# Kernel tuning notes

Measured on AMD Instinct MI355X. Metric: run time of the kernel, lower is better.

The kernel has to match this reference:

```python
import jax, jax.numpy as jnp
import numpy as np

N_U, N_I, N_B, D, L = 100000, 50000, 10, 64, 2
N_EDGES, BATCH = 1000000, 2048
DROPOUT, TEMP = 0.25, 0.2
LAMBDA_1, LAMBDA_2, LAMBDA_3 = 0.2, 0.2, 1e-7
IS_NORM = True


def setup_inputs() -> dict:
    key = jax.random.key(0)
    ks = jax.random.split(key, 10)
    E_u_0 = jax.random.normal(ks[0], (N_U, D), jnp.float32) * 0.01
    E_v_0 = jax.random.normal(ks[1], (N_I, D), jnp.float32) * 0.01
    E_b = jax.random.normal(ks[2], (N_B, D), jnp.float32) * 0.01
    adj_vals = jax.random.uniform(ks[3], (N_EDGES,), jnp.float32) * 0.05
    adj_rows = jax.random.randint(ks[4], (N_EDGES,), 0, N_U, jnp.int32)
    adj_cols = jax.random.randint(ks[5], (N_EDGES,), 0, N_I, jnp.int32)
    uids = jax.random.randint(ks[6], (BATCH,), 0, N_U, jnp.int32)
    iids = jax.random.randint(ks[7], (BATCH,), 0, N_I, jnp.int32)
    pos = jax.random.randint(ks[8], (BATCH,), 0, N_I, jnp.int32)
    neg = jax.random.randint(ks[9], (BATCH,), 0, N_I, jnp.int32)
    return {"E_u_0": E_u_0, "E_v_0": E_v_0, "E_b": E_b, "adj_vals": adj_vals,
            "adj_rows": adj_rows, "adj_cols": adj_cols,
            "uids": uids, "iids": iids, "pos": pos, "neg": neg}


def _sparse_dropout(key, vals):
    # fresh Bernoulli mask + inverted-dropout rescale on the sparse values
    keep = jax.random.bernoulli(key, 1.0 - DROPOUT, vals.shape)
    return jnp.where(keep, vals / (1.0 - DROPOUT), jnp.zeros_like(vals))


def _propagate(Eu0, Ev0, vals, rows, cols, base_key):
    # L layers of bipartite spmm: Eu <- A @ Ev ; Ev <- A.T @ Eu (fresh dropout each spmm)
    Eu, Ev = Eu0, Ev0
    Eu_sum, Ev_sum = Eu0, Ev0
    for layer in range(L):
        v1 = _sparse_dropout(jax.random.fold_in(base_key, 2 * layer), vals)
        v2 = _sparse_dropout(jax.random.fold_in(base_key, 2 * layer + 1), vals)
        Eu_new = jax.ops.segment_sum(v1[:, None] * Ev[cols], rows, num_segments=Eu0.shape[0])
        Ev_new = jax.ops.segment_sum(v2[:, None] * Eu[rows], cols, num_segments=Ev0.shape[0])
        Eu, Ev = Eu_new, Ev_new
        Eu_sum = Eu_sum + Eu
        Ev_sum = Ev_sum + Ev
    return Eu_sum, Ev_sum


def reference(E_u_0, E_v_0, E_b, adj_vals, adj_rows, adj_cols, uids, iids, pos, neg):
    drop_key = jax.random.key(42)
    # base graph propagation
    E_u, E_v = _propagate(E_u_0, E_v_0, adj_vals, adj_rows, adj_cols,
                          jax.random.fold_in(drop_key, 0))
    # learned edge weights -> augmented graph (detached, elementwise * adj_norm)
    edge_logits = jnp.sum(E_u[adj_rows] * E_v[adj_cols], axis=1)  # [E]
    Ag = jax.nn.sigmoid(edge_logits)
    aug_vals = jax.lax.stop_gradient(Ag) * adj_vals
    Z_u, Z_i = _propagate(E_u_0, E_v_0, aug_vals, adj_rows, adj_cols,
                          jax.random.fold_in(drop_key, 1))
    # BPR loss
    u_emb, pos_emb, neg_emb = E_u[uids], E_v[pos], E_v[neg]
    pos_scores = jnp.sum(u_emb * pos_emb, axis=-1)
    neg_scores = jnp.sum(u_emb * neg_emb, axis=-1)
    loss_bpr = -jnp.mean(jnp.log(jax.nn.sigmoid(pos_scores - neg_scores)))
    # PCL (InfoNCE between augmented and base views)
    neg_s = jnp.mean(jnp.log(jnp.sum(jnp.exp(Z_u[uids] @ E_u.T / TEMP), axis=1) + 1e-8))
    neg_s = neg_s + jnp.mean(jnp.log(jnp.sum(jnp.exp(Z_i[iids] @ E_v.T / TEMP), axis=1) + 1e-8))
    pos_s = jnp.mean(jnp.clip(jnp.sum(Z_u[uids] * E_u[uids], axis=1) / TEMP, -5.0, 5.0))
    pos_s = pos_s + jnp.mean(jnp.clip(jnp.sum(Z_i[iids] * E_v[iids], axis=1) / TEMP, -5.0, 5.0))
    loss_pcl = neg_s - pos_s
    # BCL (bucketed contrastive loss; is_norm=True, is_mean=False)
    if IS_NORM:
        weight_b = (pos_scores - pos_scores.min()) / (pos_scores.max() - pos_scores.min() + 1e-9)
    else:
        weight_b = jax.nn.sigmoid(pos_scores)
    relations = jnp.clip((weight_b * N_B).astype(jnp.int32), 0, N_B - 1)  # [B]
    el = jax.nn.sigmoid(E_u[uids] * E_v[pos])                              # [B, D]
    xb = E_b[relations]                                                    # [B, D]
    mask = 1.0 - jax.nn.one_hot(relations, N_B, dtype=el.dtype)            # [B, N_B]
    neg_bcl = jnp.mean(jnp.mean((el @ E_b.T) * mask, axis=-1))
    pos_bcl = jnp.mean(jnp.sum(el * xb, axis=-1))
    loss_bcl = neg_bcl - pos_bcl
    # L2 reg over parameters
    loss_reg = LAMBDA_3 * (jnp.sum(E_u_0 ** 2) + jnp.sum(E_v_0 ** 2) + jnp.sum(E_b ** 2))
    loss = loss_bpr + LAMBDA_1 * loss_pcl + LAMBDA_2 * loss_bcl + loss_reg
    return jnp.stack([loss, loss_bpr, LAMBDA_1 * loss_pcl, LAMBDA_2 * loss_bcl])
```

## Files before the change

### kernel.cpp

```cpp
#include <hip/hip_runtime.h>
#include <stdint.h>

#define NU 100000
#define NI 50000
#define NBK 10
#define DD 64
#define NE 1000000
#define BATCH 2048
#define NSLICE 8
#define USLICE ((NU + NSLICE - 1) / NSLICE)
#define ISLICE ((NI + NSLICE - 1) / NSLICE)
#define NCHUNK 512
#define EPC ((NE + NCHUNK - 1) / NCHUNK)
#define CAP_U 32
#define CAP_I 64
#define FP8_SCALE 128.0f
#define SPMM_DESCALE (1.0f / 96.0f)
#define EL_DESCALE (1.0f / 16384.0f)
#define LOG2E5 7.2134752f
#define AV_ENC 40960.0f
#define AV_DEC (0.05f / 2048.0f)
#define AUG_ENC (65535.0f / 0.05f)
#define AUG_DEC (0.05f / 65535.0f)

typedef __bf16 bf16x8 __attribute__((ext_vector_type(8)));
typedef float f32x4 __attribute__((ext_vector_type(4)));
typedef float f32x2 __attribute__((ext_vector_type(2)));
typedef unsigned long long u64x2 __attribute__((ext_vector_type(2)));

struct Keys8 { uint32_t k[8][2]; };

__host__ __device__ inline void tf2x32(uint32_t k0, uint32_t k1, uint32_t x0, uint32_t x1,
                                       uint32_t& o0, uint32_t& o1) {
  uint32_t ks0 = k0, ks1 = k1, ks2 = k0 ^ k1 ^ 0x1BD11BDAu;
  x0 += ks0; x1 += ks1;
#define TFR(r) { x0 += x1; x1 = (x1 << (r)) | (x1 >> (32 - (r))); x1 ^= x0; }
  TFR(13) TFR(15) TFR(26) TFR(6)   x0 += ks1; x1 += ks2 + 1u;
  TFR(17) TFR(29) TFR(16) TFR(24)  x0 += ks2; x1 += ks0 + 2u;
  TFR(13) TFR(15) TFR(26) TFR(6)   x0 += ks0; x1 += ks1 + 3u;
  TFR(17) TFR(29) TFR(16) TFR(24)  x0 += ks1; x1 += ks2 + 4u;
  TFR(13) TFR(15) TFR(26) TFR(6)   x0 += ks2; x1 += ks0 + 5u;
#undef TFR
  o0 = x0; o1 = x1;
}

__device__ inline uint16_t f2bf(float f) {
  uint32_t u = __float_as_uint(f);
  return (uint16_t)((u + 0x7fffu + ((u >> 16) & 1u)) >> 16);
}
__device__ inline float bf2f(uint16_t u) {
  return __uint_as_float(((uint32_t)u) << 16);
}

__device__ inline uint32_t mm_enc(float f) {
  uint32_t s = __float_as_uint(f);
  return (s & 0x80000000u) ? ~s : (s | 0x80000000u);
}
__device__ inline float mm_dec(uint32_t u) {
  uint32_t s = (u & 0x80000000u) ? (u ^ 0x80000000u) : ~u;
  return __uint_as_float(s);
}

template <int SEL>
__device__ inline float fp8_sel(uint32_t w) {
#if __has_builtin(__builtin_amdgcn_cvt_f32_fp8)
  return __builtin_amdgcn_cvt_f32_fp8((int)w, SEL);
#else
  uint32_t b = (w >> (8 * SEL)) & 0xFFu;
  uint32_t s = b >> 7, e = (b >> 3) & 0xF, m = b & 7;
  float v = (e == 0) ? (float)m * (1.0f / 512.0f)
                     : __uint_as_float(((e + 120) << 23) | (m << 20));
  return s ? -v : v;
#endif
}
__device__ inline f32x4 fp8_to4(uint32_t w) {
#if __has_builtin(__builtin_amdgcn_cvt_pk_f32_fp8)
  f32x2 lo = __builtin_amdgcn_cvt_pk_f32_fp8((int)w, false);
  f32x2 hi = __builtin_amdgcn_cvt_pk_f32_fp8((int)w, true);
  f32x4 r; r[0] = lo[0]; r[1] = lo[1]; r[2] = hi[0]; r[3] = hi[1];
  return r;
#else
  f32x4 r; r[0] = fp8_sel<0>(w); r[1] = fp8_sel<1>(w);
  r[2] = fp8_sel<2>(w); r[3] = fp8_sel<3>(w);
  return r;
#endif
}
__device__ inline uint32_t f32_to_fp8(float f) {
#if __has_builtin(__builtin_amdgcn_cvt_pk_fp8_f32)
  return (uint32_t)__builtin_amdgcn_cvt_pk_fp8_f32(f, f, 0, false) & 0xFFu;
#else
  uint32_t s = (__float_as_uint(f) >> 31) << 7;
  float a = fabsf(f);
  a = fminf(a, 448.0f);
  if (a < 0.015625f) {
    uint32_t m = (uint32_t)(a * 512.0f + 0.5f);
    return s | m;
  }
  int ex; float fr = frexpf(a, &ex);
  uint32_t q = (uint32_t)(fr * 16.0f + 0.5f);
  int E = ex + 6;
  if (q == 16) { q = 8; E += 1; }
  if (E > 15) { E = 15; q = 14; }
  if (E == 15 && q == 15) q = 14;
  return s | ((uint32_t)E << 3) | (q - 8);
#endif
}
__device__ inline uint32_t pack4_fp8(float a, float b, float c, float d) {
  return f32_to_fp8(a) | (f32_to_fp8(b) << 8) | (f32_to_fp8(c) << 16) | (f32_to_fp8(d) << 24);
}

__device__ inline uint64_t pack_edge(int r, int c, uint32_t m, float a) {
  uint32_t q = (uint32_t)(a * AV_ENC + 0.5f);
  if (q > 2047u) q = 2047u;
  return (uint64_t)(uint32_t)r | ((uint64_t)(uint32_t)c << 17) |
         ((uint64_t)m << 33) | ((uint64_t)q << 41);
}

#define CVTB 2048
#define MASKB ((NE / 2 + 255) / 256)
#define ZEROB ((NU + NI + 255) / 256)

__global__ void prep_kernel(const float4* __restrict__ a, int na4,
                            uint32_t* __restrict__ oca, uint32_t* __restrict__ oia,
                            const float4* __restrict__ b, int nb4,
                            uint32_t* __restrict__ ocb, uint32_t* __restrict__ oib,
                            const float4* __restrict__ c, int nc4,
                            float* __restrict__ acc,
                            const int* __restrict__ rows, const int* __restrict__ cols,
                            const float* __restrict__ av,
                            uint64_t* __restrict__ pk, Keys8 K,
                            int* __restrict__ cnt, uint32_t* __restrict__ mmi) {
  int bid = blockIdx.x, tid = threadIdx.x;
  if (bid < CVTB) {
    __shared__ float red[256];
    int total = na4 + nb4 + nc4;
    float s = 0.f;
    for (int i = bid * 256 + tid; i < total; i += CVTB * 256) {
      float4 v = (i < na4) ? a[i] : (i < na4 + nb4) ? b[i - na4] : c[i - na4 - nb4];
      s += v.x * v.x + v.y * v.y + v.z * v.z + v.w * v.w;
      if (i < na4 + nb4) {
        uint32_t w = pack4_fp8(v.x * FP8_SCALE, v.y * FP8_SCALE, v.z * FP8_SCALE, v.w * FP8_SCALE);
        if (i < na4) {
          oca[i] = w;
          oia[((i >> 4) << 5) + ((i & 15) << 1)] = w;
        } else {
          int j = i - na4;
          ocb[j] = w;
          oib[((j >> 4) << 5) + ((j & 15) << 1)] = w;
        }
      }
    }
    red[tid] = s;
    __syncthreads();
    for (int st = 128; st > 0; st >>= 1) {
      if (tid < st) red[tid] += red[tid + st];
      __syncthreads();
    }
    if (tid == 0) atomicAdd(&acc[7], red[0]);
  } else if (bid < CVTB + MASKB) {
    const int half = NE / 2;
    int e = (bid - CVTB) * 256 + tid;
    if (e >= half) return;
    uint32_t mlo = 0, mhi = 0;
#pragma unroll
    for (int j = 0; j < 8; ++j) {
      uint32_t o0, o1;
      tf2x32(K.k[j][0], K.k[j][1], (uint32_t)e, (uint32_t)(e + half), o0, o1);
      float u0 = __uint_as_float((o0 >> 9) | 0x3f800000u) - 1.0f;
      float u1 = __uint_as_float((o1 >> 9) | 0x3f800000u) - 1.0f;
      mlo |= (u0 < 0.75f ? 1u : 0u) << j;
      mhi |= (u1 < 0.75f ? 1u : 0u) << j;
    }
    pk[e] = pack_edge(rows[e], cols[e], mlo, av[e]);
    pk[e + half] = pack_edge(rows[e + half], cols[e + half], mhi, av[e + half]);
  } else {
    int i = (bid - CVTB - MASKB) * 256 + tid;
    if (i < NU + NI) cnt[i] = 0;
    if (i == 0) { mmi[0] = 0xFFFFFFFFu; mmi[1] = 0u; }
  }
}

__global__ __launch_bounds__(256)
void scatter_kernel(const uint64_t* __restrict__ pk,
                    int* __restrict__ cntU, int* __restrict__ cntI,
                    int* __restrict__ cpU, int* __restrict__ cpI) {
  int slice = blockIdx.x & 7;
  int chunk = blockIdx.x >> 3;
  int base = chunk * EPC;
  int end = base + EPC; if (end > NE) end = NE;
  for (int e = base + 2 * (int)threadIdx.x; e < end; e += 512) {
    u64x2 pp = __builtin_nontemporal_load((const u64x2*)(pk + e));
    uint64_t p0 = pp[0], p1 = pp[1];
    int r0 = (int)(p0 & 0x1FFFFu), r1 = (int)(p1 & 0x1FFFFu);
    int c0 = (int)((p0 >> 17) & 0xFFFFu), c1 = (int)((p1 >> 17) & 0xFFFFu);
    uint32_t m0 = (uint32_t)(p0 >> 33) & 0xFFu, m1 = (uint32_t)(p1 >> 33) & 0xFFu;
    uint32_t q0 = ((uint32_t)(p0 >> 41) & 0x7FFu) << 21;
    uint32_t q1 = ((uint32_t)(p1 >> 41) & 0x7FFu) << 21;
    if (r0 / USLICE == slice) {
      int old = atomicAdd(&cntU[r0], 1);
      cpU[(r0 << 5) + old] = (int)((uint32_t)c0 | ((m0 & 0xFu) << 17) | q0);
    }
    if (r1 / USLICE == slice) {
      int old = atomicAdd(&cntU[r1], 1);
      cpU[(r1 << 5) + old] = (int)((uint32_t)c1 | ((m1 & 0xFu) << 17) | q1);
    }
    if (c0 / ISLICE == slice) {
      int old = atomicAdd(&cntI[c0], 1);
      cpI[(c0 << 6) + old] = (int)((uint32_t)r0 | (((m0 >> 4) & 0xFu) << 17) | q0);
    }
    if (c1 / ISLICE == slice) {
      int old = atomicAdd(&cntI[c1], 1);
      cpI[(c1 << 6) + old] = (int)((uint32_t)r1 | (((m1 >> 4) & 0xFu) << 17) | q1);
    }
  }
}

__device__ inline float cp_weight(int cc, const uint16_t* __restrict__ rdw, int p, int shift) {
  float mb = (float)((cc >> shift) & 1);
  if (rdw) return (float)rdw[p] * AUG_DEC * mb;
  return (float)(((uint32_t)cc) >> 21) * AV_DEC * mb;
}

__global__ __launch_bounds__(256)
void spmm_layer_kernel(const int* __restrict__ cntU, const int* __restrict__ cpU,
                       const int* __restrict__ cntI, const int* __restrict__ cpI,
                       const uint16_t* __restrict__ rdU, const uint16_t* __restrict__ rdI,
                       int shift,
                       const uint8_t* __restrict__ SU, const uint8_t* __restrict__ SI,
                       uint8_t* __restrict__ dU, uint8_t* __restrict__ dI,
                       uint16_t* __restrict__ sumU, uint16_t* __restrict__ sumI,
                       const float* __restrict__ baseU, const float* __restrict__ baseI,
                       uint8_t* __restrict__ s8U, uint8_t* __restrict__ s8I) {
  int lane = threadIdx.x & 63;
  int g = lane >> 4, l15 = lane & 15;
  int w = (blockIdx.x * blockDim.x + threadIdx.x) >> 6;
  int r = w * 4 + g;
  const int* cnt; const int* cp; const uint8_t* S; const uint16_t* rdw;
  uint8_t* D; uint16_t* Sum; const float* base; uint8_t* S8; int row, cap;
  if (r < NU) {
    row = r; cnt = cntU; cp = cpU; S = SU; rdw = rdU; cap = CAP_U;
    D = dU; Sum = sumU; base = baseU; S8 = s8U;
  } else {
    row = r - NU; cnt = cntI; cp = cpI; S = SI; rdw = rdI; cap = CAP_I;
    D = dI; Sum = sumI; base = baseI; S8 = s8I;
  }
  int p0 = row * cap, p1 = p0 + cnt[row];
  f32x4 acc = {0.f, 0.f, 0.f, 0.f};
  int p = p0;
  for (; p + 4 <= p1; p += 4) {
    int c0 = cp[p], c1 = cp[p + 1], c2 = cp[p + 2], c3 = cp[p + 3];
    float v0 = cp_weight(c0, rdw, p, shift);
    float v1 = cp_weight(c1, rdw, p + 1, shift);
    float v2 = cp_weight(c2, rdw, p + 2, shift);
    float v3 = cp_weight(c3, rdw, p + 3, shift);
    uint32_t a0 = (v0 != 0.f) ? (uint32_t)(c0 & 0x1FFFF) : 0u;
    uint32_t a1 = (v1 != 0.f) ? (uint32_t)(c1 & 0x1FFFF) : 0u;
    uint32_t a2 = (v2 != 0.f) ? (uint32_t)(c2 & 0x1FFFF) : 0u;
    uint32_t a3 = (v3 != 0.f) ? (uint32_t)(c3 & 0x1FFFF) : 0u;
    uint32_t w0 = *(const uint32_t*)(S + ((size_t)a0 << 6) + l15 * 4);
    uint32_t w1 = *(const uint32_t*)(S + ((size_t)a1 << 6) + l15 * 4);
    uint32_t w2 = *(const uint32_t*)(S + ((size_t)a2 << 6) + l15 * 4);
    uint32_t w3 = *(const uint32_t*)(S + ((size_t)a3 << 6) + l15 * 4);
    f32x4 f0 = fp8_to4(w0), f1 = fp8_to4(w1), f2 = fp8_to4(w2), f3 = fp8_to4(w3);
#pragma unroll
    for (int k = 0; k < 4; ++k)
      acc[k] += (v0 * f0[k] + v1 * f1[k]) + (v2 * f2[k] + v3 * f3[k]);
  }
  for (; p < p1; ++p) {
    int c0 = cp[p];
    float v0 = cp_weight(c0, rdw, p, shift);
    if (v0 != 0.f) {
      uint32_t w0 = *(const uint32_t*)(S + ((size_t)(uint32_t)(c0 & 0x1FFFF) << 6) + l15 * 4);
      f32x4 f0 = fp8_to4(w0);
#pragma unroll
      for (int k = 0; k < 4; ++k) acc[k] += v0 * f0[k];
    }
  }
  size_t idx = (size_t)row * DD + l15 * 4;
  if (D) {
    *(uint32_t*)(D + idx) = pack4_fp8(acc[0] * (4.0f / 3.0f), acc[1] * (4.0f / 3.0f),
                                      acc[2] * (4.0f / 3.0f), acc[3] * (4.0f / 3.0f));
    float4 b4 = *(const float4*)(base + idx);
    ushort4 s;
    s.x = f2bf(b4.x + acc[0] * SPMM_DESCALE);
    s.y = f2bf(b4.y + acc[1] * SPMM_DESCALE);
    s.z = f2bf(b4.z + acc[2] * SPMM_DESCALE);
    s.w = f2bf(b4.w + acc[3] * SPMM_DESCALE);
    *(ushort4*)(Sum + idx) = s;
  } else {
    ushort4 s = *(const ushort4*)(Sum + idx);
    float s0 = bf2f(s.x) + acc[0] * SPMM_DESCALE;
    float s1 = bf2f(s.y) + acc[1] * SPMM_DESCALE;
    float s2 = bf2f(s.z) + acc[2] * SPMM_DESCALE;
    float s3 = bf2f(s.w) + acc[3] * SPMM_DESCALE;
    s.x = f2bf(s0); s.y = f2bf(s1); s.z = f2bf(s2); s.w = f2bf(s3);
    *(ushort4*)(Sum + idx) = s;
    if (S8)
      *(uint32_t*)(S8 + ((size_t)row << 7) + l15 * 8 + 4) =
          pack4_fp8(s0 * FP8_SCALE, s1 * FP8_SCALE, s2 * FP8_SCALE, s3 * FP8_SCALE);
  }
}

__global__ __launch_bounds__(256)
void spmm_aug_kernel(const int* __restrict__ cntU, const int* __restrict__ cpU,
                     const int* __restrict__ cntI, const int* __restrict__ cpI,
                     const uint8_t* __restrict__ TU, const uint8_t* __restrict__ TI,
                     uint8_t* __restrict__ dU, uint8_t* __restrict__ dI,
                     uint16_t* __restrict__ sumU, uint16_t* __restrict__ sumI,
                     const float* __restrict__ baseU, const float* __restrict__ baseI,
                     uint16_t* __restrict__ wrU, uint16_t* __restrict__ wrI) {
  int lane = threadIdx.x & 63;
  int g = lane >> 4, l15 = lane & 15;
  int w = (blockIdx.x * blockDim.x + threadIdx.x) >> 6;
  int r = w * 4 + g;
  const int* cnt; const int* cp; const uint8_t *T, *Rt;
  uint8_t* D; uint16_t* Sum; const float* base; uint16_t* wr; int row, cap;
  if (r < NU) {
    row = r; cnt = cntU; cp = cpU; T = TI; Rt = TU; cap = CAP_U;
    D = dU; Sum = sumU; base = baseU; wr = wrU;
  } else {
    row = r - NU; cnt = cntI; cp = cpI; T = TU; Rt = TI; cap = CAP_I;
    D = dI; Sum = sumI; base = baseI; wr = wrI;
  }
  uint32_t rv = *(const uint32_t*)(Rt + ((size_t)row << 7) + l15 * 8 + 4);
  f32x4 rr = fp8_to4(rv);
  int p0 = row * cap, p1 = p0 + cnt[row];
  f32x4 acc = {0.f, 0.f, 0.f, 0.f};
  int p = p0;
  for (; p + 4 <= p1; p += 4) {
    int c0 = cp[p], c1 = cp[p + 1], c2 = cp[p + 2], c3 = cp[p + 3];
    uint2 sg0 = *(const uint2*)(T + ((size_t)(uint32_t)(c0 & 0x1FFFF) << 7) + l15 * 8);
    uint2 sg1 = *(const uint2*)(T + ((size_t)(uint32_t)(c1 & 0x1FFFF) << 7) + l15 * 8);
    uint2 sg2 = *(const uint2*)(T + ((size_t)(uint32_t)(c2 & 0x1FFFF) << 7) + l15 * 8);
    uint2 sg3 = *(const uint2*)(T + ((size_t)(uint32_t)(c3 & 0x1FFFF) << 7) + l15 * 8);
    f32x4 g0 = fp8_to4(sg0.y), g1 = fp8_to4(sg1.y);
    f32x4 g2 = fp8_to4(sg2.y), g3 = fp8_to4(sg3.y);
    float d0 = rr[0] * g0[0] + rr[1] * g0[1] + rr[2] * g0[2] + rr[3] * g0[3];
    float d1 = rr[0] * g1[0] + rr[1] * g1[1] + rr[2] * g1[2] + rr[3] * g1[3];
    float d2 = rr[0] * g2[0] + rr[1] * g2[1] + rr[2] * g2[2] + rr[3] * g2[3];
    float d3 = rr[0] * g3[0] + rr[1] * g3[1] + rr[2] * g3[2] + rr[3] * g3[3];
#pragma unroll
    for (int o = 1; o < 16; o <<= 1) {
      d0 += __shfl_xor(d0, o, 16);
      d1 += __shfl_xor(d1, o, 16);
      d2 += __shfl_xor(d2, o, 16);
      d3 += __shfl_xor(d3, o, 16);
    }
    float a0 = (float)(((uint32_t)c0) >> 21) * AV_DEC / (1.0f + __expf(-d0 * EL_DESCALE));
    float a1 = (float)(((uint32_t)c1) >> 21) * AV_DEC / (1.0f + __expf(-d1 * EL_DESCALE));
    float a2 = (float)(((uint32_t)c2) >> 21) * AV_DEC / (1.0f + __expf(-d2 * EL_DESCALE));
    float a3 = (float)(((uint32_t)c3) >> 21) * AV_DEC / (1.0f + __expf(-d3 * EL_DESCALE));
    if (l15 == 0) {
      wr[p] = (uint16_t)(a0 * AUG_ENC + 0.5f);
      wr[p + 1] = (uint16_t)(a1 * AUG_ENC + 0.5f);
      wr[p + 2] = (uint16_t)(a2 * AUG_ENC + 0.5f);
      wr[p + 3] = (uint16_t)(a3 * AUG_ENC + 0.5f);
    }
    float v0 = a0 * (float)((c0 >> 19) & 1);
    float v1 = a1 * (float)((c1 >> 19) & 1);
    float v2 = a2 * (float)((c2 >> 19) & 1);
    float v3 = a3 * (float)((c3 >> 19) & 1);
    f32x4 f0 = fp8_to4(sg0.x), f1 = fp8_to4(sg1.x);
    f32x4 f2 = fp8_to4(sg2.x), f3 = fp8_to4(sg3.x);
#pragma unroll
    for (int k = 0; k < 4; ++k)
      acc[k] += (v0 * f0[k] + v1 * f1[k]) + (v2 * f2[k] + v3 * f3[k]);
  }
  for (; p < p1; ++p) {
    int c0 = cp[p];
    uint2 sg0 = *(const uint2*)(T + ((size_t)(uint32_t)(c0 & 0x1FFFF) << 7) + l15 * 8);
    f32x4 g0 = fp8_to4(sg0.y);
    float d0 = rr[0] * g0[0] + rr[1] * g0[1] + rr[2] * g0[2] + rr[3] * g0[3];
#pragma unroll
    for (int o = 1; o < 16; o <<= 1) d0 += __shfl_xor(d0, o, 16);
    float a0 = (float)(((uint32_t)c0) >> 21) * AV_DEC / (1.0f + __expf(-d0 * EL_DESCALE));
    if (l15 == 0) wr[p] = (uint16_t)(a0 * AUG_ENC + 0.5f);
    float v0 = a0 * (float)((c0 >> 19) & 1);
    f32x4 f0 = fp8_to4(sg0.x);
#pragma unroll
    for (int k = 0; k < 4; ++k) acc[k] += v0 * f0[k];
  }
  size_t idx = (size_t)row * DD + l15 * 4;
  *(uint32_t*)(D + idx) = pack4_fp8(acc[0] * (4.0f / 3.0f), acc[1] * (4.0f / 3.0f),
                                    acc[2] * (4.0f / 3.0f), acc[3] * (4.0f / 3.0f));
  float4 b4 = *(const float4*)(base + idx);
  ushort4 s;
  s.x = f2bf(b4.x + acc[0] * SPMM_DESCALE);
  s.y = f2bf(b4.y + acc[1] * SPMM_DESCALE);
  s.z = f2bf(b4.z + acc[2] * SPMM_DESCALE);
  s.w = f2bf(b4.w + acc[3] * SPMM_DESCALE);
  *(ushort4*)(Sum + idx) = s;
}

__global__ __launch_bounds__(256)
void pcl_mfma9_kernel(const uint16_t* __restrict__ Zgu, const uint16_t* __restrict__ E16u,
                      int NTu, float* __restrict__ Su,
                      const uint16_t* __restrict__ Zgi, const uint16_t* __restrict__ E16i,
                      int NTi, float* __restrict__ Si) {
  __shared__ uint8_t ldsb[2][2048];
  int lane = threadIdx.x & 63;
  int wave = threadIdx.x >> 6;
  int quad = lane >> 4, l15 = lane & 15;
  bool isU = blockIdx.y < 8;
  const uint16_t* Zg = isU ? Zgu : Zgi;
  const uint16_t* E16 = isU ? E16u : E16i;
  int NT = isU ? NTu : NTi;
  float* S = isU ? Su : Si;
  const int SPL = 128;
  int mt0 = (((int)blockIdx.y & 7) * 4 + wave) * 4;
  bf16x8 a0[4], a1[4];
#pragma unroll
  for (int i = 0; i < 4; ++i) {
    const uint16_t* ar = Zg + (size_t)((mt0 + i) * 16 + l15) * 64 + quad * 8;
    a0[i] = *(const bf16x8*)ar;
    a1[i] = *(const bf16x8*)(ar + 32);
  }
  int t = threadIdx.x;
  int wof = (t * 8) ^ (((t >> 4) & 7) << 4);
  int rof0 = (l15 * 128 + quad * 16) ^ ((l15 & 7) << 4);
  int rof1 = (l15 * 128 + quad * 16 + 64) ^ ((l15 & 7) << 4);
  f32x4 rs[4] = {};
  int nt = blockIdx.x;
  {
    uint2 g0 = make_uint2(0u, 0u);
    if (nt < NT)
      g0 = *(const uint2*)((const uint8_t*)E16 + (size_t)nt * 2048 + t * 8);
    *(uint2*)(&ldsb[0][wof]) = g0;
  }
  __syncthreads();
  int cur = 0;
  while (nt < NT) {
    int nn = nt + SPL;
    uint2 gn = make_uint2(0u, 0u);
    if (nn < NT)
      gn = *(const uint2*)((const uint8_t*)E16 + (size_t)nn * 2048 + t * 8);
    bf16x8 b0 = *(const bf16x8*)(&ldsb[cur][rof0]);
    bf16x8 b1 = *(const bf16x8*)(&ldsb[cur][rof1]);
#pragma unroll
    for (int i = 0; i < 4; ++i) {
      f32x4 c = {0.f, 0.f, 0.f, 0.f};
      c = __builtin_amdgcn_mfma_f32_16x16x32_bf16(a0[i], b0, c, 0, 0, 0);
      c = __builtin_amdgcn_mfma_f32_16x16x32_bf16(a1[i], b1, c, 0, 0, 0);
#pragma unroll
      for (int r = 0; r < 4; ++r) rs[i][r] += __builtin_amdgcn_exp2f(c[r]);
    }
    *(uint2*)(&ldsb[cur ^ 1][wof]) = gn;
    __syncthreads();
    cur ^= 1; nt = nn;
  }
#pragma unroll
  for (int off = 8; off > 0; off >>= 1) {
#pragma unroll
    for (int i = 0; i < 4; ++i)
#pragma unroll
      for (int r = 0; r < 4; ++r) rs[i][r] += __shfl_down(rs[i][r], off, 16);
  }
  if (l15 == 0) {
#pragma unroll
    for (int i = 0; i < 4; ++i)
#pragma unroll
      for (int r = 0; r < 4; ++r)
        atomicAdd(&S[(mt0 + i) * 16 + quad * 4 + r], rs[i][r]);
  }
}

__global__ __launch_bounds__(256)
void post_kernel(const uint16_t* __restrict__ Z16u, const uint16_t* __restrict__ Z16i,
                 const uint16_t* __restrict__ E16u, const uint16_t* __restrict__ E16i,
                 const int* __restrict__ uids, const int* __restrict__ iids,
                 const int* __restrict__ pos, const int* __restrict__ neg,
                 uint16_t* __restrict__ Zgu, uint16_t* __restrict__ Zgi,
                 float* __restrict__ ps, float* __restrict__ acc,
                 uint32_t* __restrict__ mmi) {
  int bid = blockIdx.x, tid = threadIdx.x;
  int lane = tid & 63;
  if (bid < 1024) {
    int row = bid * 4 + (tid >> 6);
    if (row < BATCH)
      Zgu[(size_t)row * 64 + lane] = f2bf(bf2f(Z16u[(size_t)uids[row] * 64 + lane]) * LOG2E5);
    else {
      int bb = row - BATCH;
      Zgi[(size_t)bb * 64 + lane] = f2bf(bf2f(Z16i[(size_t)iids[bb] * 64 + lane]) * LOG2E5);
    }
  } else if (bid < 1536) {
    int b = ((bid - 1024) * 256 + tid) >> 6;
    if (b >= BATCH) return;
    float u = bf2f(E16u[(size_t)uids[b] * DD + lane]);
    float p = u * bf2f(E16i[(size_t)pos[b] * DD + lane]);
    float n = u * bf2f(E16i[(size_t)neg[b] * DD + lane]);
#pragma unroll
    for (int off = 32; off > 0; off >>= 1) { p += __shfl_down(p, off); n += __shfl_down(n, off); }
    if (lane == 0) {
      ps[b] = p;
      uint32_t eu = mm_enc(p);
      atomicMin(&mmi[0], eu);
      atomicMax(&mmi[1], eu);
      float x = p - n;
      atomicAdd(&acc[0], logf(1.0f / (1.0f + __expf(-x))));
    }
  } else {
    int b = ((bid - 1536) * 256 + tid) >> 6;
    if (b >= 2 * BATCH) return;
    const uint16_t *Z, *E; const int* ids; int idx, bb;
    if (b < BATCH) { Z = Z16u; E = E16u; ids = uids; idx = 3; bb = b; }
    else { Z = Z16i; E = E16i; ids = iids; idx = 4; bb = b - BATCH; }
    size_t r = (size_t)ids[bb] * DD + lane;
    float p = bf2f(Z[r]) * bf2f(E[r]);
#pragma unroll
    for (int off = 32; off > 0; off >>= 1) p += __shfl_down(p, off);
    if (lane == 0) {
      float x = p * 5.0f;
      x = fminf(5.0f, fmaxf(-5.0f, x));
      atomicAdd(&acc[idx], x);
    }
  }
}

__global__ void bcl_kernel(const uint16_t* __restrict__ E16u, const uint16_t* __restrict__ E16i,
                           const float* __restrict__ Eb, const int* __restrict__ uids,
                           const int* __restrict__ pos, const float* __restrict__ ps,
                           const uint32_t* __restrict__ mmi, float* __restrict__ acc) {
  int lane = threadIdx.x & 63;
  int b = (blockIdx.x * blockDim.x + threadIdx.x) >> 6;
  if (b >= BATCH) return;
  float mn = mm_dec(mmi[0]);
  float mx = mm_dec(mmi[1]);
  float wgt = (ps[b] - mn) / (mx - mn + 1e-9f);
  int rel = (int)(wgt * 10.0f);
  rel = rel < 0 ? 0 : (rel > 9 ? 9 : rel);
  float x = bf2f(E16u[(size_t)uids[b] * DD + lane]) * bf2f(E16i[(size_t)pos[b] * DD + lane]);
  float el = 1.0f / (1.0f + __expf(-x));
  float sneg = 0.f, spos = 0.f;
  for (int k = 0; k < NBK; ++k) {
    float d = el * Eb[k * DD + lane];
#pragma unroll
    for (int off = 32; off > 0; off >>= 1) d += __shfl_down(d, off);
    if (lane == 0) { if (k == rel) spos = d; else sneg += d; }
  }
  if (lane == 0) {
    atomicAdd(&acc[5], sneg * 0.1f);
    atomicAdd(&acc[6], spos);
  }
}

__global__ void finalize_kernel(const float* __restrict__ Su, const float* __restrict__ Si,
                                const float* __restrict__ acc, float* __restrict__ out) {
  __shared__ float r1[256], r2[256];
  int tid = threadIdx.x;
  float su = 0.f, si = 0.f;
  for (int b = tid; b < BATCH; b += 256) {
    su += logf(Su[b] + 1e-8f);
    si += logf(Si[b] + 1e-8f);
  }
  r1[tid] = su; r2[tid] = si;
  __syncthreads();
  for (int s = 128; s > 0; s >>= 1) {
    if (tid < s) { r1[tid] += r1[tid + s]; r2[tid] += r2[tid + s]; }
    __syncthreads();
  }
  if (tid == 0) {
    const float inv = 1.0f / (float)BATCH;
    float neg_s = (r1[0] + r2[0]) * inv;
    float pos_s = (acc[3] + acc[4]) * inv;
    float pcl = neg_s - pos_s;
    float bpr = -acc[0] * inv;
    float bcl = (acc[5] - acc[6]) * inv;
    float reg = 1e-7f * acc[7];
    float loss = bpr + 0.2f * pcl + 0.2f * bcl + reg;
    out[0] = loss; out[1] = bpr; out[2] = 0.2f * pcl; out[3] = 0.2f * bcl;
  }
}

extern "C" void kernel_launch(void* const* d_in, const int* in_sizes, int n_in,
                              void* d_out, int out_size, void* d_ws, size_t ws_size,
                              hipStream_t stream) {
  (void)in_sizes; (void)n_in; (void)out_size; (void)ws_size;
  const float* Eu0 = (const float*)d_in[0];
  const float* Ev0 = (const float*)d_in[1];
  const float* Eb  = (const float*)d_in[2];
  const float* av  = (const float*)d_in[3];
  const int* rows  = (const int*)d_in[4];
  const int* cols  = (const int*)d_in[5];
  const int* uids  = (const int*)d_in[6];
  const int* iids  = (const int*)d_in[7];
  const int* pos   = (const int*)d_in[8];
  const int* neg   = (const int*)d_in[9];
  float* out = (float*)d_out;

  float* w = (float*)d_ws;
  size_t o = 0;
  float* ps  = w + o; o += BATCH;
  float* Su  = w + o; o += BATCH;
  float* Si  = w + o; o += BATCH;
  float* acc = w + o; o += 16;
  uint32_t* mmi = (uint32_t*)(w + o); o += 2;
  uint16_t* hp = (uint16_t*)(w + o);
  uint16_t* E16u = hp; hp += (size_t)NU * DD;
  uint16_t* E16i = hp; hp += (size_t)NI * DD;
  uint16_t* Z16u = hp; hp += (size_t)NU * DD;
  uint16_t* Z16i = hp; hp += (size_t)NI * DD;
  uint16_t* Zgu  = hp; hp += (size_t)BATCH * DD;
  uint16_t* Zgi  = hp; hp += (size_t)BATCH * DD;
  uint16_t* augU = hp; hp += (size_t)NU * CAP_U + 64;
  uint16_t* augI = hp; hp += (size_t)NI * CAP_I + 64;
  uint8_t* bp = (uint8_t*)hp;
  uint8_t* TU  = bp; bp += (size_t)NU * 128;
  uint8_t* TI  = bp; bp += (size_t)NI * 128;
  uint8_t* E0u8 = bp; bp += (size_t)NU * DD;
  uint8_t* E0v8 = bp; bp += (size_t)NI * DD;
  uint8_t* d8U = bp; bp += (size_t)NU * DD;
  uint8_t* d8I = bp; bp += (size_t)NI * DD;
  uint8_t* qp = (uint8_t*)(((uintptr_t)bp + 127) & ~(uintptr_t)127);
  uint64_t* pk = (uint64_t*)qp; qp += (size_t)NE * 8;
  int* ip = (int*)qp;
  int* cntU = ip; ip += NU;
  int* cntI = ip; ip += NI;
  int* cpU = ip; ip += (size_t)NU * CAP_U;
  int* cpI = ip; ip += (size_t)NI * CAP_I;

  uint32_t bk[2][2];
  tf2x32(0u, 42u, 0u, 0u, bk[0][0], bk[0][1]);
  tf2x32(0u, 42u, 0u, 1u, bk[1][0], bk[1][1]);
  Keys8 K;
  for (int p = 0; p < 2; ++p)
    for (int l = 0; l < 2; ++l) {
      tf2x32(bk[p][0], bk[p][1], 0u, (uint32_t)(2 * l),     K.k[p * 2 + l][0], K.k[p * 2 + l][1]);
      tf2x32(bk[p][0], bk[p][1], 0u, (uint32_t)(2 * l + 1), K.k[4 + p * 2 + l][0], K.k[4 + p * 2 + l][1]);
    }

  (void)hipMemsetAsync(ps, 0, (3 * BATCH + 18) * sizeof(float), stream);
  prep_kernel<<<CVTB + MASKB + ZEROB, 256, 0, stream>>>(
      (const float4*)Eu0, NU * DD / 4, (uint32_t*)E0u8, (uint32_t*)TU,
      (const float4*)Ev0, NI * DD / 4, (uint32_t*)E0v8, (uint32_t*)TI,
      (const float4*)Eb, NBK * DD / 4, acc, rows, cols, av, pk, K, cntU, mmi);
  scatter_kernel<<<NCHUNK * NSLICE, 256, 0, stream>>>(pk, cntU, cntI, cpU, cpI);

  const int SPB = (NU + NI) / 16;

  spmm_layer_kernel<<<SPB, 256, 0, stream>>>(cntU, cpU, cntI, cpI, nullptr, nullptr, 17,
                                             E0v8, E0u8, d8U, d8I,
                                             E16u, E16i, Eu0, Ev0, nullptr, nullptr);
  spmm_layer_kernel<<<SPB, 256, 0, stream>>>(cntU, cpU, cntI, cpI, nullptr, nullptr, 18,
                                             d8I, d8U, nullptr, nullptr,
                                             E16u, E16i, nullptr, nullptr, TU, TI);

  spmm_aug_kernel<<<SPB, 256, 0, stream>>>(cntU, cpU, cntI, cpI, TU, TI,
                                           d8U, d8I, Z16u, Z16i, Eu0, Ev0,
                                           augU, augI);
  spmm_layer_kernel<<<SPB, 256, 0, stream>>>(cntU, cpU, cntI, cpI, augU, augI, 20,
                                             d8I, d8U, nullptr, nullptr,
                                             Z16u, Z16i, nullptr, nullptr, nullptr, nullptr);

  post_kernel<<<2560, 256, 0, stream>>>(Z16u, Z16i, E16u, E16i, uids, iids, pos, neg,
                                        Zgu, Zgi, ps, acc, mmi);

  bcl_kernel<<<BATCH / 4, 256, 0, stream>>>(E16u, E16i, Eb, uids, pos, ps, mmi, acc);

  pcl_mfma9_kernel<<<dim3(128, 16), 256, 0, stream>>>(Zgu, E16u, NU / 16, Su,
                                                      Zgi, E16i, NI / 16, Si);

  finalize_kernel<<<1, 256, 0, stream>>>(Su, Si, acc, out);
}
```

Baseline: 668.7 us.

## Pre-bin edges into per-slice lists during prep instead of rescanning all edges per slice

```diff
diff --git a/kernel.cpp b/kernel.cpp
--- a/kernel.cpp
+++ b/kernel.cpp
@@ -10,10 +10,9 @@
 #define NSLICE 8
 #define USLICE ((NU + NSLICE - 1) / NSLICE)
 #define ISLICE ((NI + NSLICE - 1) / NSLICE)
-#define NCHUNK 512
-#define EPC ((NE + NCHUNK - 1) / NCHUNK)
 #define CAP_U 32
 #define CAP_I 64
+#define LISTCAP 133120
 #define FP8_SCALE 128.0f
 #define SPMM_DESCALE (1.0f / 96.0f)
 #define EL_DESCALE (1.0f / 16384.0f)
@@ -26,7 +25,6 @@
 typedef __bf16 bf16x8 __attribute__((ext_vector_type(8)));
 typedef float f32x4 __attribute__((ext_vector_type(4)));
 typedef float f32x2 __attribute__((ext_vector_type(2)));
-typedef unsigned long long u64x2 __attribute__((ext_vector_type(2)));
 
 struct Keys8 { uint32_t k[8][2]; };
 
@@ -109,13 +107,6 @@
   return f32_to_fp8(a) | (f32_to_fp8(b) << 8) | (f32_to_fp8(c) << 16) | (f32_to_fp8(d) << 24);
 }
 
-__device__ inline uint64_t pack_edge(int r, int c, uint32_t m, float a) {
-  uint32_t q = (uint32_t)(a * AV_ENC + 0.5f);
-  if (q > 2047u) q = 2047u;
-  return (uint64_t)(uint32_t)r | ((uint64_t)(uint32_t)c << 17) |
-         ((uint64_t)m << 33) | ((uint64_t)q << 41);
-}
-
 #define CVTB 2048
 #define MASKB ((NE / 2 + 255) / 256)
 #define ZEROB ((NU + NI + 255) / 256)
@@ -128,7 +119,7 @@
                             float* __restrict__ acc,
                             const int* __restrict__ rows, const int* __restrict__ cols,
                             const float* __restrict__ av,
-                            uint64_t* __restrict__ pk, Keys8 K,
+                            uint64_t* __restrict__ lists, int* __restrict__ tails, Keys8 K,
                             int* __restrict__ cnt, uint32_t* __restrict__ mmi) {
   int bid = blockIdx.x, tid = threadIdx.x;
   if (bid < CVTB) {
@@ -158,21 +149,56 @@
     }
     if (tid == 0) atomicAdd(&acc[7], red[0]);
   } else if (bid < CVTB + MASKB) {
+    __shared__ int lcnt[16];
+    __shared__ int lbase[16];
+    if (tid < 16) lcnt[tid] = 0;
+    __syncthreads();
     const int half = NE / 2;
     int e = (bid - CVTB) * 256 + tid;
-    if (e >= half) return;
-    uint32_t mlo = 0, mhi = 0;
-#pragma unroll
-    for (int j = 0; j < 8; ++j) {
-      uint32_t o0, o1;
-      tf2x32(K.k[j][0], K.k[j][1], (uint32_t)e, (uint32_t)(e + half), o0, o1);
-      float u0 = __uint_as_float((o0 >> 9) | 0x3f800000u) - 1.0f;
-      float u1 = __uint_as_float((o1 >> 9) | 0x3f800000u) - 1.0f;
-      mlo |= (u0 < 0.75f ? 1u : 0u) << j;
-      mhi |= (u1 < 0.75f ? 1u : 0u) << j;
-    }
-    pk[e] = pack_edge(rows[e], cols[e], mlo, av[e]);
-    pk[e + half] = pack_edge(rows[e + half], cols[e + half], mhi, av[e + half]);
+    bool act = (e < half);
+    int r0 = 0, c0 = 0, r1 = 0, c1 = 0;
+    uint32_t cpu0 = 0, cpi0 = 0, cpu1 = 0, cpi1 = 0;
+    int su0 = 0, si0 = 8, su1 = 0, si1 = 8;
+    int tu0 = 0, ti0 = 0, tu1 = 0, ti1 = 0;
+    if (act) {
+      uint32_t mlo = 0, mhi = 0;
+#pragma unroll
+      for (int j = 0; j < 8; ++j) {
+        uint32_t o0, o1;
+        tf2x32(K.k[j][0], K.k[j][1], (uint32_t)e, (uint32_t)(e + half), o0, o1);
+        float u0 = __uint_as_float((o0 >> 9) | 0x3f800000u) - 1.0f;
+        float u1 = __uint_as_float((o1 >> 9) | 0x3f800000u) - 1.0f;
+        mlo |= (u0 < 0.75f ? 1u : 0u) << j;
+        mhi |= (u1 < 0.75f ? 1u : 0u) << j;
+      }
+      r0 = rows[e]; c0 = cols[e];
+      r1 = rows[e + half]; c1 = cols[e + half];
+      uint32_t q0 = (uint32_t)(av[e] * AV_ENC + 0.5f); if (q0 > 2047u) q0 = 2047u;
+      uint32_t q1 = (uint32_t)(av[e + half] * AV_ENC + 0.5f); if (q1 > 2047u) q1 = 2047u;
+      cpu0 = (uint32_t)c0 | ((mlo & 0xFu) << 17) | (q0 << 21);
+      cpi0 = (uint32_t)r0 | (((mlo >> 4) & 0xFu) << 17) | (q0 << 21);
+      cpu1 = (uint32_t)c1 | ((mhi & 0xFu) << 17) | (q1 << 21);
+      cpi1 = (uint32_t)r1 | (((mhi >> 4) & 0xFu) << 17) | (q1 << 21);
+      su0 = r0 / USLICE; si0 = 8 + c0 / ISLICE;
+      su1 = r1 / USLICE; si1 = 8 + c1 / ISLICE;
+      tu0 = atomicAdd(&lcnt[su0], 1);
+      ti0 = atomicAdd(&lcnt[si0], 1);
+      tu1 = atomicAdd(&lcnt[su1], 1);
+      ti1 = atomicAdd(&lcnt[si1], 1);
+    }
+    __syncthreads();
+    if (tid < 16) lbase[tid] = (lcnt[tid] > 0) ? atomicAdd(&tails[tid], lcnt[tid]) : 0;
+    __syncthreads();
+    if (act) {
+      lists[(size_t)su0 * LISTCAP + lbase[su0] + tu0] =
+          (uint64_t)(uint32_t)r0 | ((uint64_t)cpu0 << 32);
+      lists[(size_t)si0 * LISTCAP + lbase[si0] + ti0] =
+          (uint64_t)(uint32_t)c0 | ((uint64_t)cpi0 << 32);
+      lists[(size_t)su1 * LISTCAP + lbase[su1] + tu1] =
+          (uint64_t)(uint32_t)r1 | ((uint64_t)cpu1 << 32);
+      lists[(size_t)si1 * LISTCAP + lbase[si1] + ti1] =
+          (uint64_t)(uint32_t)c1 | ((uint64_t)cpi1 << 32);
+    }
   } else {
     int i = (bid - CVTB - MASKB) * 256 + tid;
     if (i < NU + NI) cnt[i] = 0;
@@ -181,37 +207,23 @@
 }
 
 __global__ __launch_bounds__(256)
-void scatter_kernel(const uint64_t* __restrict__ pk,
+void scatter_kernel(const uint64_t* __restrict__ lists, const int* __restrict__ tails,
                     int* __restrict__ cntU, int* __restrict__ cntI,
                     int* __restrict__ cpU, int* __restrict__ cpI) {
-  int slice = blockIdx.x & 7;
-  int chunk = blockIdx.x >> 3;
-  int base = chunk * EPC;
-  int end = base + EPC; if (end > NE) end = NE;
-  for (int e = base + 2 * (int)threadIdx.x; e < end; e += 512) {
-    u64x2 pp = __builtin_nontemporal_load((const u64x2*)(pk + e));
-    uint64_t p0 = pp[0], p1 = pp[1];
-    int r0 = (int)(p0 & 0x1FFFFu), r1 = (int)(p1 & 0x1FFFFu);
-    int c0 = (int)((p0 >> 17) & 0xFFFFu), c1 = (int)((p1 >> 17) & 0xFFFFu);
-    uint32_t m0 = (uint32_t)(p0 >> 33) & 0xFFu, m1 = (uint32_t)(p1 >> 33) & 0xFFu;
-    uint32_t q0 = ((uint32_t)(p0 >> 41) & 0x7FFu) << 21;
-    uint32_t q1 = ((uint32_t)(p1 >> 41) & 0x7FFu) << 21;
-    if (r0 / USLICE == slice) {
-      int old = atomicAdd(&cntU[r0], 1);
-      cpU[(r0 << 5) + old] = (int)((uint32_t)c0 | ((m0 & 0xFu) << 17) | q0);
-    }
-    if (r1 / USLICE == slice) {
-      int old = atomicAdd(&cntU[r1], 1);
-      cpU[(r1 << 5) + old] = (int)((uint32_t)c1 | ((m1 & 0xFu) << 17) | q1);
-    }
-    if (c0 / ISLICE == slice) {
-      int old = atomicAdd(&cntI[c0], 1);
-      cpI[(c0 << 6) + old] = (int)((uint32_t)r0 | (((m0 >> 4) & 0xFu) << 17) | q0);
-    }
-    if (c1 / ISLICE == slice) {
-      int old = atomicAdd(&cntI[c1], 1);
-      cpI[(c1 << 6) + old] = (int)((uint32_t)r1 | (((m1 >> 4) & 0xFu) << 17) | q1);
-    }
+  int list = blockIdx.x & 15;
+  int chunk = blockIdx.x >> 4;
+  const uint64_t* L = lists + (size_t)list * LISTCAP;
+  int len = tails[list];
+  bool isU = list < 8;
+  int* cnt = isU ? cntU : cntI;
+  int* cp  = isU ? cpU  : cpI;
+  int sh   = isU ? 5 : 6;
+  for (int i = chunk * 256 + (int)threadIdx.x; i < len; i += 256 * 256) {
+    uint64_t en = __builtin_nontemporal_load(L + i);
+    int row = (int)(uint32_t)en;
+    int val = (int)(uint32_t)(en >> 32);
+    int old = atomicAdd(&cnt[row], 1);
+    cp[(row << sh) + old] = val;
   }
 }
 
@@ -594,6 +606,7 @@
   float* Si  = w + o; o += BATCH;
   float* acc = w + o; o += 16;
   uint32_t* mmi = (uint32_t*)(w + o); o += 2;
+  int* tails = (int*)(w + o); o += 16;
   uint16_t* hp = (uint16_t*)(w + o);
   uint16_t* E16u = hp; hp += (size_t)NU * DD;
   uint16_t* E16i = hp; hp += (size_t)NI * DD;
@@ -611,7 +624,7 @@
   uint8_t* d8U = bp; bp += (size_t)NU * DD;
   uint8_t* d8I = bp; bp += (size_t)NI * DD;
   uint8_t* qp = (uint8_t*)(((uintptr_t)bp + 127) & ~(uintptr_t)127);
-  uint64_t* pk = (uint64_t*)qp; qp += (size_t)NE * 8;
+  uint64_t* lists = (uint64_t*)qp; qp += (size_t)16 * LISTCAP * 8;
   int* ip = (int*)qp;
   int* cntU = ip; ip += NU;
   int* cntI = ip; ip += NI;
@@ -628,12 +641,12 @@
       tf2x32(bk[p][0], bk[p][1], 0u, (uint32_t)(2 * l + 1), K.k[4 + p * 2 + l][0], K.k[4 + p * 2 + l][1]);
     }
 
-  (void)hipMemsetAsync(ps, 0, (3 * BATCH + 18) * sizeof(float), stream);
+  (void)hipMemsetAsync(ps, 0, (3 * BATCH + 34) * sizeof(float), stream);
   prep_kernel<<<CVTB + MASKB + ZEROB, 256, 0, stream>>>(
       (const float4*)Eu0, NU * DD / 4, (uint32_t*)E0u8, (uint32_t*)TU,
       (const float4*)Ev0, NI * DD / 4, (uint32_t*)E0v8, (uint32_t*)TI,
-      (const float4*)Eb, NBK * DD / 4, acc, rows, cols, av, pk, K, cntU, mmi);
-  scatter_kernel<<<NCHUNK * NSLICE, 256, 0, stream>>>(pk, cntU, cntI, cpU, cpI);
+      (const float4*)Eb, NBK * DD / 4, acc, rows, cols, av, lists, tails, K, cntU, mmi);
+  scatter_kernel<<<4096, 256, 0, stream>>>(lists, tails, cntU, cntI, cpU, cpI);
 
   const int SPB = (NU + NI) / 16;
 
```

After: 670.1 us. No clear change (+0.2%).
